# Optimization experiments

Measured on AMD Instinct MI355X. Metric: run time of the kernel, lower is better.

Reference implementation:

```python
import jax, jax.numpy as jnp
import numpy as np

B, S, D = 2, 2048, 4096
H, KVH, HD = 32, 8, 128
MULT = 0.08838834764831845  # 1/sqrt(head_dim)
MAXV = 30.0                 # tanh soft-cap
ROPE_BASE = 10000.0


def _rope_cos_sin(position_ids, hd=HD, base=ROPE_BASE):
    inv_freq = 1.0 / (base ** (jnp.arange(0, hd, 2, dtype=jnp.float32) / hd))
    freqs = position_ids.astype(jnp.float32)[..., None] * inv_freq  # [B,S,hd/2]
    emb = jnp.concatenate([freqs, freqs], axis=-1)                  # [B,S,hd]
    return jnp.cos(emb), jnp.sin(emb)


def _rotate_half(x):
    half = x.shape[-1] // 2
    return jnp.concatenate([-x[..., half:], x[..., :half]], axis=-1)


def setup_inputs() -> dict:
    key = jax.random.key(0)
    ks = jax.random.split(key, 5)
    hidden_states = jax.random.normal(ks[0], (B, S, D), dtype=jnp.float32)
    position_ids = jnp.broadcast_to(jnp.arange(S, dtype=jnp.int64), (B, S))
    # True = masked (causal upper triangle)
    causal = jnp.triu(jnp.ones((S, S), dtype=bool), k=1)
    attention_mask = jnp.broadcast_to(causal, (B, 1, S, S))
    sc = 0.02
    q_w = jax.random.normal(ks[1], (D, H * HD), dtype=jnp.float32) * sc
    k_w = jax.random.normal(ks[2], (D, KVH * HD), dtype=jnp.float32) * sc
    v_w = jax.random.normal(ks[3], (D, KVH * HD), dtype=jnp.float32) * sc
    o_w = jax.random.normal(ks[4], (H * HD, D), dtype=jnp.float32) * sc
    return {"hidden_states": hidden_states, "position_ids": position_ids,
            "attention_mask": attention_mask, "q_w": q_w, "k_w": k_w,
            "v_w": v_w, "o_w": o_w}


def reference(hidden_states, position_ids, attention_mask, q_w, k_w, v_w, o_w):
    bsz, q_len, _ = hidden_states.shape
    q = (hidden_states @ q_w).reshape(bsz, q_len, H, HD).transpose(0, 2, 1, 3)    # [B,H,S,HD]
    k = (hidden_states @ k_w).reshape(bsz, q_len, KVH, HD).transpose(0, 2, 1, 3)  # [B,KVH,S,HD]
    v = (hidden_states @ v_w).reshape(bsz, q_len, KVH, HD).transpose(0, 2, 1, 3)

    cos, sin = _rope_cos_sin(position_ids)   # [B,S,HD]
    cos = cos[:, None]                       # [B,1,S,HD]
    sin = sin[:, None]
    q = q * cos + _rotate_half(q) * sin
    k = k * cos + _rotate_half(k) * sin

    groups = H // KVH
    k = jnp.repeat(k, groups, axis=1)        # [B,H,S,HD]
    v = jnp.repeat(v, groups, axis=1)

    scores = jnp.einsum('bhqd,bhkd->bhqk', q, k).astype(jnp.float32) * MULT
    scores = MAXV * jnp.tanh(scores / MAXV)
    scores = jnp.where(attention_mask, jnp.float32(-10000.0), scores)
    attn = jax.nn.softmax(scores, axis=-1).astype(q.dtype)

    out = jnp.einsum('bhqk,bhkd->bhqd', attn, v)       # [B,H,S,HD]
    out = out.transpose(0, 2, 1, 3).reshape(bsz, q_len, H * HD)
    return out @ o_w
```

## Files before the change

kernel.cpp:

```cpp
#include <hip/hip_runtime.h>
#include <stdint.h>

#define B_ 2
#define S_ 2048
#define D_ 4096
#define H_ 32
#define KVH_ 8
#define HD_ 128
#define GRP_ (H_/KVH_)
#define NQKV 6144
#define MULT_ 0.08838834764831845f
#define MAXV_ 30.0f

typedef __attribute__((ext_vector_type(8))) short s16x8;
typedef __attribute__((ext_vector_type(4))) float fx4;

__device__ __forceinline__ unsigned short f2bf(float f) {
  unsigned int u = __float_as_uint(f);
  u += 0x7fffu + ((u >> 16) & 1u);
  return (unsigned short)(u >> 16);
}
__device__ __forceinline__ float bf2f(unsigned short h) {
  return __uint_as_float(((unsigned int)h) << 16);
}

__device__ __forceinline__ void gld_lds16(const void* g, void* l) {
  __builtin_amdgcn_global_load_lds(
      (const __attribute__((address_space(1))) unsigned int*)g,
      (__attribute__((address_space(3))) unsigned int*)l, 16, 0, 0);
}


__global__ void k_f2bf(const float* __restrict__ src, unsigned short* __restrict__ dst, int n4) {
  int i = blockIdx.x * blockDim.x + threadIdx.x;
  int stride = gridDim.x * blockDim.x;
  for (; i < n4; i += stride) {
    float4 v = ((const float4*)src)[i];
    ushort4 o;
    o.x = f2bf(v.x); o.y = f2bf(v.y); o.z = f2bf(v.z); o.w = f2bf(v.w);
    ((ushort4*)dst)[i] = o;
  }
}

__global__ void k_transpose_w(const float* __restrict__ src, int ncols,
                              unsigned short* __restrict__ dst) {
  __shared__ float tile[32][33];
  int k0 = blockIdx.x * 32;
  int n0 = blockIdx.y * 32;
  int tx = threadIdx.x, ty = threadIdx.y;
  for (int i = 0; i < 32; i += 8)
    tile[ty + i][tx] = src[(size_t)(k0 + ty + i) * ncols + n0 + tx];
  __syncthreads();
  for (int i = 0; i < 32; i += 8)
    dst[(size_t)(n0 + ty + i) * 4096 + k0 + tx] = f2bf(tile[tx][ty + i]);
}

__global__ void k_transpose_v(const unsigned short* __restrict__ qkv,
                              unsigned short* __restrict__ vt) {
  __shared__ unsigned short tile[32][33];
  int s0 = blockIdx.x * 32;
  int d0 = blockIdx.y * 32;
  int bk = blockIdx.z;
  int b = bk / KVH_, kvh = bk % KVH_;
  int tx = threadIdx.x, ty = threadIdx.y;
  for (int i = 0; i < 32; i += 8)
    tile[ty + i][tx] = qkv[(size_t)(b*S_ + s0 + ty + i)*NQKV + 5120 + kvh*HD_ + d0 + tx];
  __syncthreads();
  for (int i = 0; i < 32; i += 8)
    vt[((size_t)bk*HD_ + d0 + ty + i)*S_ + s0 + tx] = tile[tx][ty + i];
}

__global__ void k_rope(const unsigned short* __restrict__ qkv,
                       unsigned short* __restrict__ Q, unsigned short* __restrict__ K) {
  int bs = blockIdx.x;
  int b = bs >> 11;
  int s = bs & (S_ - 1);
  __shared__ float cs[64], sn[64];
  int t = threadIdx.x;
  if (t < 64) {
    float inv = __expf(-(float)t * 0.14391156831212787f);
    float fr = (float)s * inv;
    cs[t] = cosf(fr); sn[t] = sinf(fr);
  }
  __syncthreads();
  const unsigned short* row = qkv + (size_t)bs * NQKV;
  for (int i = t; i < H_*HD_; i += 256) {
    int h = i >> 7, d = i & 127;
    float x = bf2f(row[i]);
    float x2, c, si;
    if (d < 64) { x2 = -bf2f(row[h*128 + d + 64]); c = cs[d];    si = sn[d]; }
    else        { x2 =  bf2f(row[h*128 + d - 64]); c = cs[d-64]; si = sn[d-64]; }
    Q[((size_t)(b*H_ + h)*S_ + s)*HD_ + d] = f2bf(x*c + x2*si);
  }
  for (int i = t; i < KVH_*HD_; i += 256) {
    int h = i >> 7, d = i & 127;
    float x = bf2f(row[4096 + i]);
    float x2, c, si;
    if (d < 64) { x2 = -bf2f(row[4096 + h*128 + d + 64]); c = cs[d];    si = sn[d]; }
    else        { x2 =  bf2f(row[4096 + h*128 + d - 64]); c = cs[d-64]; si = sn[d-64]; }
    K[((size_t)(b*KVH_ + h)*S_ + s)*HD_ + d] = f2bf(x*c + x2*si);
  }
}

#define BAR() asm volatile("s_barrier" ::: "memory")
#define SB0() __builtin_amdgcn_sched_barrier(0)


#define STG4(buf, isB, h, kt) do {                                           \
  const unsigned short* _src = (isB) ? Bt : A;                               \
  size_t _rb = (size_t)(((isB) ? bn : bm)*((isB) ? 128 : 256)                \
                        + (h)*((isB) ? 64 : 128));                           \
  _Pragma("unroll") for (int _rr = 0; _rr < ((isB) ? 1 : 2); ++_rr) {        \
    int _s = _rr*8 + wv;                                                     \
    gld_lds16(_src + (_rb + (size_t)((_s>>1)*16))*Kd                         \
                   + (size_t)((kt)*64 + (_s&1)*32) + lane_off,               \
              ldsc + (buf)*49152 + (isB)*32768                               \
                   + (h)*((isB) ? 8192 : 16384) + _s*1024);                  \
  }                                                                          \
} while (0)

#define LDA4(buf, mh) do {                                                   \
  _Pragma("unroll") for (int _i = 0; _i < 4; ++_i)                           \
  _Pragma("unroll") for (int _kk = 0; _kk < 2; ++_kk)                        \
    Afr[_i*2+_kk] = *(const s16x8*)(ldsc + (buf)*49152 + wr*16384            \
                    + ((((mh)*4+_i)*2+_kk)*1024) + aswz);                    \
} while (0)

#define LDB4(buf) do {                                                       \
  _Pragma("unroll") for (int _nf = 0; _nf < 2; ++_nf)                        \
  _Pragma("unroll") for (int _kk = 0; _kk < 2; ++_kk) {                      \
    int _r0 = wc*32 + _nf*16;                                                \
    Bfr[_nf*2+_kk] = *(const s16x8*)(ldsc + (buf)*49152 + 32768              \
                    + (_r0>>6)*8192 + ((((_r0&63)>>4)*2+_kk)*1024) + aswz);  \
  }                                                                          \
} while (0)

#define MFMA16(MH) do {                                                      \
  __builtin_amdgcn_s_setprio(1);                                            \
  _Pragma("unroll") for (int _i = 0; _i < 4; ++_i)                           \
  _Pragma("unroll") for (int _nf = 0; _nf < 2; ++_nf)                        \
  _Pragma("unroll") for (int _kk = 0; _kk < 2; ++_kk)                        \
    acc[(MH)*4+_i][_nf] = __builtin_amdgcn_mfma_f32_16x16x32_bf16(           \
        Afr[_i*2+_kk], Bfr[_nf*2+_kk], acc[(MH)*4+_i][_nf], 0, 0, 0);        \
  __builtin_amdgcn_s_setprio(0);                                            \
} while (0)

#define VMC2() asm volatile("s_waitcnt vmcnt(2)" ::: "memory")

__global__ __launch_bounds__(512, 2)
void k_gemm4(const unsigned short* __restrict__ A, const unsigned short* __restrict__ Bt,
             unsigned short* __restrict__ C, int Kdim, int N, int MB) {
  __shared__ __align__(16) char ldsbuf[98304];
  char* ldsc = ldsbuf;
  const size_t Kd = (size_t)Kdim;
  const int NT = Kdim >> 6;

  int nwg = gridDim.x;
  int flat = blockIdx.x;
  int q = nwg >> 3, r8 = nwg & 7, xcd = flat & 7, off = flat >> 3;
  int wg = (xcd < r8 ? xcd*(q+1) : r8*(q+1) + (xcd-r8)*q) + off;
  int bm = wg % MB, bn = wg / MB;

  int tid = threadIdx.x;
  int lane = tid & 63, wv = tid >> 6;
  int wr = wv >> 2, wc = wv & 3;
  int l15 = lane & 15, l4 = lane >> 4;
  const int aswz = (l15 << 6) + ((l4 << 4) ^ ((l15 & 8) ? 32 : 0));
  const size_t lane_off = (size_t)(lane >> 2) * Kd
                        + (size_t)(((lane & 3) << 3) ^ ((lane & 32) >> 1));

  fx4 acc[8][2] = {};
  s16x8 Afr[8], Bfr[4];

  STG4(0, 0, 0, 0); STG4(0, 0, 1, 0);
  STG4(0, 1, 0, 0); STG4(0, 1, 1, 0);
  STG4(1, 1, 0, 1); STG4(1, 1, 1, 1);
  VMC2();
  BAR();

  for (int t2 = 0; t2 < NT; t2 += 2) {
    int tb1 = t2 + 1;
    int tn0 = t2 + 2; if (tn0 >= NT) tn0 -= NT;
    int tn1 = t2 + 3; if (tn1 >= NT) tn1 -= NT;
    LDA4(0, 0); LDB4(0);
    STG4(1, 0, 0, tb1); STG4(1, 0, 1, tb1);
    BAR();
    MFMA16(0);
    SB0(); BAR();
    LDA4(0, 1);
    STG4(0, 1, 0, tn0); STG4(0, 1, 1, tn0);
    BAR();
    MFMA16(1);
    SB0(); VMC2(); BAR();
    LDA4(1, 0); LDB4(1);
    STG4(0, 0, 0, tn0); STG4(0, 0, 1, tn0);
    BAR();
    MFMA16(0);
    SB0(); BAR();
    LDA4(1, 1);
    STG4(1, 1, 0, tn1); STG4(1, 1, 1, tn1);
    BAR();
    MFMA16(1);
    SB0(); VMC2(); BAR();
  }

  int m0 = bm*256 + wr*128 + l4*4;
#pragma unroll
  for (int af = 0; af < 8; ++af)
#pragma unroll
    for (int nf = 0; nf < 2; ++nf)
#pragma unroll
      for (int r = 0; r < 4; ++r) {
        int m = m0 + af*16 + r;
        int n = bn*128 + wc*32 + nf*16 + l15;
        C[(size_t)m*N + n] = f2bf(acc[af][nf][r]);
      }
}


#define STAGE(buf, isB, h, kt) do {                                          \
  const unsigned short* _src = (isB) ? Bt : A;                               \
  size_t _rb = (size_t)(((isB) ? bn : bm)*256 + (h)*128);                    \
  _Pragma("unroll") for (int _rr = 0; _rr < 2; ++_rr) {                      \
    int _s = _rr*8 + wv;                                                     \
    gld_lds16(_src + (_rb + (size_t)((_s>>1)*16))*Kd                         \
                   + (size_t)((kt)*64 + (_s&1)*32) + lane_off,               \
              ldsc + (buf)*65536 + (isB)*32768 + (h)*16384 + _s*1024);       \
  }                                                                          \
} while (0)

#define LDA(dst, buf, mh) do {                                               \
  _Pragma("unroll") for (int _i = 0; _i < 4; ++_i)                           \
  _Pragma("unroll") for (int _kk = 0; _kk < 2; ++_kk)                        \
    dst[_i*2+_kk] = *(const s16x8*)(ldsc + (buf)*65536 + wr*16384            \
                    + ((((mh)*4+_i)*2+_kk)*1024) + aswz);                    \
} while (0)

#define LDB(dst, buf, nh) do {                                               \
  _Pragma("unroll") for (int _j = 0; _j < 2; ++_j)                           \
  _Pragma("unroll") for (int _kk = 0; _kk < 2; ++_kk)                        \
    dst[_j*2+_kk] = *(const s16x8*)(ldsc + (buf)*65536 + 32768               \
                    + (wc>>1)*16384                                          \
                    + ((((wc&1)*4+(nh)*2+_j)*2+_kk)*1024) + aswz);           \
} while (0)

#define MFMA_Q(Aa, Bb, MH, NH) do {                                          \
  __builtin_amdgcn_s_setprio(1);                                            \
  _Pragma("unroll") for (int _i = 0; _i < 4; ++_i)                           \
  _Pragma("unroll") for (int _j = 0; _j < 2; ++_j)                           \
  _Pragma("unroll") for (int _kk = 0; _kk < 2; ++_kk)                        \
    acc[(MH)*4+_i][(NH)*2+_j] = __builtin_amdgcn_mfma_f32_16x16x32_bf16(     \
        Aa[_i*2+_kk], Bb[_j*2+_kk], acc[(MH)*4+_i][(NH)*2+_j], 0, 0, 0);     \
  __builtin_amdgcn_s_setprio(0);                                            \
} while (0)

#define VMC4() asm volatile("s_waitcnt vmcnt(4)" ::: "memory")

__global__ __launch_bounds__(512, 2)
void k_gemm8(const unsigned short* __restrict__ A, const unsigned short* __restrict__ Bt,
             float* __restrict__ C, int Kdim, int N, int MB) {
  __shared__ __align__(16) char ldsbuf[131072];
  char* ldsc = ldsbuf;
  const size_t Kd = (size_t)Kdim;
  const int NT = Kdim >> 6;

  int nwg = gridDim.x;
  int flat = blockIdx.x;
  int q = nwg >> 3, r8 = nwg & 7, xcd = flat & 7, off = flat >> 3;
  int wg = (xcd < r8 ? xcd*(q+1) : r8*(q+1) + (xcd-r8)*q) + off;
  int bm = wg % MB, bn = wg / MB;

  int tid = threadIdx.x;
  int lane = tid & 63, wv = tid >> 6;
  int wr = wv >> 2, wc = wv & 3;
  int l15 = lane & 15, l4 = lane >> 4;
  const int aswz = (l15 << 6) + ((l4 << 4) ^ ((l15 & 8) ? 32 : 0));
  const size_t lane_off = (size_t)(lane >> 2) * Kd
                        + (size_t)(((lane & 3) << 3) ^ ((lane & 32) >> 1));

  fx4 acc[8][4] = {};
  s16x8 Afr[8], B0fr[4], B1fr[4];

  STAGE(0, 0, 0, 0); STAGE(0, 0, 1, 0);
  STAGE(0, 1, 0, 0); STAGE(0, 1, 1, 0);
  STAGE(1, 1, 0, 1); STAGE(1, 1, 1, 1);
  VMC4();
  BAR();

  for (int t2 = 0; t2 < NT; t2 += 2) {
    int tb1 = t2 + 1;
    int tn0 = t2 + 2; if (tn0 >= NT) tn0 -= NT;
    int tn1 = t2 + 3; if (tn1 >= NT) tn1 -= NT;
    LDA(Afr, 0, 0); LDB(B0fr, 0, 0);
    STAGE(1, 0, 0, tb1);
    BAR();
    MFMA_Q(Afr, B0fr, 0, 0);
    SB0(); BAR();
    LDB(B1fr, 0, 1);
    STAGE(1, 0, 1, tb1);
    BAR();
    MFMA_Q(Afr, B1fr, 0, 1);
    SB0(); BAR();
    LDA(Afr, 0, 1);
    STAGE(0, 1, 0, tn0);
    BAR();
    MFMA_Q(Afr, B1fr, 1, 1);
    SB0(); BAR();
    STAGE(0, 1, 1, tn0);
    BAR();
    MFMA_Q(Afr, B0fr, 1, 0);
    SB0(); VMC4(); BAR();
    LDA(Afr, 1, 0); LDB(B0fr, 1, 0);
    STAGE(0, 0, 0, tn0);
    BAR();
    MFMA_Q(Afr, B0fr, 0, 0);
    SB0(); BAR();
    LDB(B1fr, 1, 1);
    STAGE(0, 0, 1, tn0);
    BAR();
    MFMA_Q(Afr, B1fr, 0, 1);
    SB0(); BAR();
    LDA(Afr, 1, 1);
    STAGE(1, 1, 0, tn1);
    BAR();
    MFMA_Q(Afr, B1fr, 1, 1);
    SB0(); BAR();
    STAGE(1, 1, 1, tn1);
    BAR();
    MFMA_Q(Afr, B0fr, 1, 0);
    SB0(); VMC4(); BAR();
  }

  int m0 = bm*256 + wr*128 + l4*4;
#pragma unroll
  for (int mf = 0; mf < 8; ++mf)
#pragma unroll
    for (int nf = 0; nf < 4; ++nf)
#pragma unroll
      for (int r = 0; r < 4; ++r) {
        int m = m0 + mf*16 + r;
        int n = bn*256 + (wc>>1)*128 + ((wc&1)*4 + nf)*16 + l15;
        C[(size_t)m*N + n] = acc[mf][nf][r];
      }
}


__global__ __launch_bounds__(256)
void k_attn8(const unsigned short* __restrict__ Q, const unsigned short* __restrict__ K,
             const unsigned short* __restrict__ Vt, unsigned short* __restrict__ Aout) {
  __shared__ unsigned short k_lds[2][32*128];
  __shared__ unsigned short v_lds[2][128*32];
  const float C1 = MULT_ * 2.0f * 1.4426950408889634f / MAXV_;
  const float C3 = 2.0f * MAXV_ * 1.4426950408889634f;
  int tpair = blockIdx.x;
  int bh = blockIdx.y;
  int b = bh >> 5, h = bh & 31;
  int kvh = h >> 2;
  int tid = threadIdx.x, lane = tid & 63, wv = tid >> 6;
  int l15 = lane & 15, l4 = lane >> 4;
  const unsigned short* Qb = Q + (size_t)bh * S_ * HD_;
  const unsigned short* Kb = K + (size_t)(b*KVH_ + kvh) * S_ * HD_;
  const unsigned short* Vb = Vt + (size_t)(b*KVH_ + kvh) * HD_ * S_;

  s16x8 ones;
#pragma unroll
  for (int i = 0; i < 8; ++i) ones[i] = (short)0x3F80;

#define STAGE_KV32(bufi, kb32) do {                                          \
  _Pragma("unroll") for (int _it = 0; _it < 2; ++_it) {                      \
    int _c = _it*256 + tid;                                                  \
    int _kr = _c >> 4;                                                       \
    int _kd = ((_c & 15) ^ (_kr & 7)) * 8;                                   \
    gld_lds16(&Kb[(size_t)((kb32) + _kr)*HD_ + _kd],                         \
              &k_lds[bufi][_it*2048 + wv*512]);                              \
    int _vd = _c >> 2;                                                       \
    int _vk = ((_c & 3) ^ (_vd & 3)) * 8;                                    \
    gld_lds16(&Vb[(size_t)_vd*S_ + (kb32) + _vk],                            \
              &v_lds[bufi][_it*2048 + wv*512]);                              \
  }                                                                          \
} while (0)

  for (int sp = 0; sp < 2; ++sp) {
    int strip = sp ? (31 - tpair) : tpair;
    int q0 = strip * 64;
    int qbase = q0 + wv * 16;
    int qr = qbase + l15;
    s16x8 bq[4];
#pragma unroll
    for (int kb = 0; kb < 4; ++kb)
      bq[kb] = *(const s16x8*)&Qb[(size_t)qr*HD_ + kb*32 + l4*8];
    fx4 oacc[8] = {};
    fx4 osum = {};
    int nt_full = qbase >> 5;
    int nt = (q0 >> 5) + 2;

    auto body = [&](int bufi, int kbase, bool domask) {
      fx4 sst[2] = {};
      __builtin_amdgcn_s_setprio(1);
#pragma unroll
      for (int nb = 0; nb < 2; ++nb)
#pragma unroll
        for (int kb = 0; kb < 4; ++kb) {
          s16x8 kf = *(const s16x8*)&k_lds[bufi][(nb*16 + l15)*128 + (((kb*4 + l4) ^ (l15 & 7)) * 8)];
          sst[nb] = __builtin_amdgcn_mfma_f32_16x16x32_bf16(kf, bq[kb], sst[nb], 0, 0, 0);
        }
      __builtin_amdgcn_s_setprio(0);
      uint32_t w[4];
#pragma unroll
      for (int nb = 0; nb < 2; ++nb) {
        float pv[4];
#pragma unroll
        for (int r = 0; r < 4; ++r) {
          float sraw = sst[nb][r];
          float e2p = __builtin_amdgcn_exp2f(sraw * C1);
          float p = __builtin_amdgcn_exp2f(-C3 * __builtin_amdgcn_rcpf(1.f + e2p));
          if (domask) {
            int kk = kbase + nb*16 + l4*4 + r;
            p = (kk <= qr) ? p : 0.f;
          }
          pv[r] = p;
        }
        w[nb*2]   = __builtin_amdgcn_perm(__float_as_uint(pv[1]), __float_as_uint(pv[0]), 0x07060302u);
        w[nb*2+1] = __builtin_amdgcn_perm(__float_as_uint(pv[3]), __float_as_uint(pv[2]), 0x07060302u);
      }
      uint32_t a0x = __shfl_xor((int)w[0], 16), a1x = __shfl_xor((int)w[1], 16);
      uint32_t b0x = __shfl_xor((int)w[2], 16), b1x = __shfl_xor((int)w[3], 16);
      bool up = (l4 & 1);
      uint32_t VA0 = up ? a0x : w[0], VA1 = up ? a1x : w[1];
      uint32_t VA2 = up ? w[0] : a0x, VA3 = up ? w[1] : a1x;
      uint32_t VB0 = up ? b0x : w[2], VB1 = up ? b1x : w[3];
      uint32_t VB2 = up ? w[2] : b0x, VB3 = up ? w[3] : b1x;
      bool lowh = (l4 < 2);
      uint32_t X0 = lowh ? VB0 : VA0, X1 = lowh ? VB1 : VA1;
      uint32_t X2 = lowh ? VB2 : VA2, X3 = lowh ? VB3 : VA3;
      uint32_t Y0 = __shfl_xor((int)X0, 32), Y1 = __shfl_xor((int)X1, 32);
      uint32_t Y2 = __shfl_xor((int)X2, 32), Y3 = __shfl_xor((int)X3, 32);
      union { uint32_t u[4]; s16x8 v; } tw;
      tw.u[0] = (l4 == 0) ? VA0 : (l4 == 3) ? VB0 : Y0;
      tw.u[1] = (l4 == 0) ? VA1 : (l4 == 3) ? VB1 : Y1;
      tw.u[2] = (l4 == 0) ? VA2 : (l4 == 3) ? VB2 : Y2;
      tw.u[3] = (l4 == 0) ? VA3 : (l4 == 3) ? VB3 : Y3;
      s16x8 pf = tw.v;
      __builtin_amdgcn_s_setprio(1);
      osum = __builtin_amdgcn_mfma_f32_16x16x32_bf16(ones, pf, osum, 0, 0, 0);
#pragma unroll
      for (int db = 0; db < 8; ++db) {
        int d = db*16 + l15;
        s16x8 vf = *(const s16x8*)&v_lds[bufi][d*32 + ((l4 ^ (d & 3)) * 8)];
        oacc[db] = __builtin_amdgcn_mfma_f32_16x16x32_bf16(vf, pf, oacc[db], 0, 0, 0);
      }
      __builtin_amdgcn_s_setprio(0);
    };

    STAGE_KV32(0, 0);
    __syncthreads();
    for (int t = 0; t < nt; ++t) {
      int bufi = t & 1;
      if (t + 1 < nt) STAGE_KV32(bufi^1, (t+1)*32);
      if (t < nt_full)       body(bufi, t*32, false);
      else if (t == nt_full) body(bufi, t*32, true);
      __syncthreads();
    }

    float rn = __builtin_amdgcn_rcpf(osum[0]);
#pragma unroll
    for (int db = 0; db < 8; ++db) {
      ushort4 o;
      o.x = f2bf(oacc[db][0] * rn);
      o.y = f2bf(oacc[db][1] * rn);
      o.z = f2bf(oacc[db][2] * rn);
      o.w = f2bf(oacc[db][3] * rn);
      *(ushort4*)&Aout[(size_t)(b*S_ + qr)*4096 + h*HD_ + db*16 + l4*4] = o;
    }
  }
#undef STAGE_KV32
}


extern "C" void kernel_launch(void* const* d_in, const int* in_sizes, int n_in,
                              void* d_out, int out_size, void* d_ws, size_t ws_size,
                              hipStream_t stream) {
  (void)in_sizes; (void)n_in; (void)out_size; (void)ws_size;
  const float* hidden = (const float*)d_in[0];
  const float* q_w = (const float*)d_in[3];
  const float* k_w = (const float*)d_in[4];
  const float* v_w = (const float*)d_in[5];
  const float* o_w = (const float*)d_in[6];
  char* ws = (char*)d_ws;
  unsigned short* hidden_bf = (unsigned short*)(ws + 0);
  unsigned short* qkv_wt    = (unsigned short*)(ws + 33554432);
  unsigned short* o_wt      = (unsigned short*)(ws + 83886080);
  unsigned short* qkv       = (unsigned short*)(ws + 117440512);
  unsigned short* Qb        = (unsigned short*)(ws + 167772160);
  unsigned short* Kb        = (unsigned short*)(ws + 201326592);
  unsigned short* Vt        = (unsigned short*)(ws + 209715200);
  unsigned short* attn_out  = (unsigned short*)(ws + 218103808);

  dim3 tb(32, 8);
  k_f2bf<<<2048, 256, 0, stream>>>(hidden, hidden_bf, (B_*S_*D_)/4);
  k_transpose_w<<<dim3(128, 128), tb, 0, stream>>>(q_w, 4096, qkv_wt);
  k_transpose_w<<<dim3(128, 32),  tb, 0, stream>>>(k_w, 1024, qkv_wt + (size_t)4096*4096);
  k_transpose_w<<<dim3(128, 32),  tb, 0, stream>>>(v_w, 1024, qkv_wt + (size_t)5120*4096);
  k_transpose_w<<<dim3(128, 128), tb, 0, stream>>>(o_w, 4096, o_wt);
  k_gemm4<<<dim3(16*48), 512, 0, stream>>>(hidden_bf, qkv_wt, qkv, D_, NQKV, 16);
  k_rope<<<B_*S_, 256, 0, stream>>>(qkv, Qb, Kb);
  k_transpose_v<<<dim3(S_/32, HD_/32, B_*KVH_), tb, 0, stream>>>(qkv, Vt);
  k_attn8<<<dim3(16, 64), 256, 0, stream>>>(Qb, Kb, Vt, attn_out);
  k_gemm8<<<dim3(16*16), 512, 0, stream>>>(attn_out, o_wt, (float*)d_out, D_, D_, 16);
}
```

Measured before the change: 582.4 us.

## Triple-buffer LDS staging in QKV projection GEMM with rotating buffers

Replaces the two-buffer, two-tiles-per-iteration pipeline of the QKV GEMM with a three-buffer LDS ring that prefetches two K-tiles ahead. Buffer indices rotate each iteration, and the wait changes to vmcnt(6), leaving one full tile of global loads in flight across the barrier. The goal is to hide more global-load latency behind the MFMA work. In exchange, LDS use grows to 144KB per block, which rules out any chance of two blocks per CU, and there is extra loop-control overhead per iteration.

```diff
diff --git a/kernel.cpp b/kernel.cpp
--- a/kernel.cpp
+++ b/kernel.cpp
@@ -104,6 +104,8 @@
 
 #define BAR() asm volatile("s_barrier" ::: "memory")
 #define SB0() __builtin_amdgcn_sched_barrier(0)
+#define VMC6() asm volatile("s_waitcnt vmcnt(6)" ::: "memory")
+#define VMC4() asm volatile("s_waitcnt vmcnt(4)" ::: "memory")
 
 
 #define STG4(buf, isB, h, kt) do {                                           \
@@ -145,12 +147,10 @@
   __builtin_amdgcn_s_setprio(0);                                            \
 } while (0)
 
-#define VMC2() asm volatile("s_waitcnt vmcnt(2)" ::: "memory")
-
 __global__ __launch_bounds__(512, 2)
-void k_gemm4(const unsigned short* __restrict__ A, const unsigned short* __restrict__ Bt,
-             unsigned short* __restrict__ C, int Kdim, int N, int MB) {
-  __shared__ __align__(16) char ldsbuf[98304];
+void k_gemm4t(const unsigned short* __restrict__ A, const unsigned short* __restrict__ Bt,
+              unsigned short* __restrict__ C, int Kdim, int N, int MB) {
+  __shared__ __align__(16) char ldsbuf[147456];
   char* ldsc = ldsbuf;
   const size_t Kd = (size_t)Kdim;
   const int NT = Kdim >> 6;
@@ -172,36 +172,25 @@
   fx4 acc[8][2] = {};
   s16x8 Afr[8], Bfr[4];
 
-  STG4(0, 0, 0, 0); STG4(0, 0, 1, 0);
-  STG4(0, 1, 0, 0); STG4(0, 1, 1, 0);
-  STG4(1, 1, 0, 1); STG4(1, 1, 1, 1);
-  VMC2();
+  STG4(0, 0, 0, 0); STG4(0, 0, 1, 0); STG4(0, 1, 0, 0); STG4(0, 1, 1, 0);
+  STG4(1, 0, 0, 1); STG4(1, 0, 1, 1); STG4(1, 1, 0, 1); STG4(1, 1, 1, 1);
+  VMC6();
   BAR();
 
-  for (int t2 = 0; t2 < NT; t2 += 2) {
-    int tb1 = t2 + 1;
-    int tn0 = t2 + 2; if (tn0 >= NT) tn0 -= NT;
-    int tn1 = t2 + 3; if (tn1 >= NT) tn1 -= NT;
-    LDA4(0, 0); LDB4(0);
-    STG4(1, 0, 0, tb1); STG4(1, 0, 1, tb1);
+  int r0 = 0, r1 = 1, r2 = 2;
+  for (int t = 0; t < NT; ++t) {
+    int tp2 = t + 2; if (tp2 >= NT) tp2 -= NT;
+    LDA4(r0, 0); LDB4(r0);
+    STG4(r2, 0, 0, tp2); STG4(r2, 0, 1, tp2);
     BAR();
     MFMA16(0);
     SB0(); BAR();
-    LDA4(0, 1);
-    STG4(0, 1, 0, tn0); STG4(0, 1, 1, tn0);
+    LDA4(r0, 1);
+    STG4(r2, 1, 0, tp2); STG4(r2, 1, 1, tp2);
     BAR();
     MFMA16(1);
-    SB0(); VMC2(); BAR();
-    LDA4(1, 0); LDB4(1);
-    STG4(0, 0, 0, tn0); STG4(0, 0, 1, tn0);
-    BAR();
-    MFMA16(0);
-    SB0(); BAR();
-    LDA4(1, 1);
-    STG4(1, 1, 0, tn1); STG4(1, 1, 1, tn1);
-    BAR();
-    MFMA16(1);
-    SB0(); VMC2(); BAR();
+    SB0(); VMC6(); BAR();
+    int tmp = r0; r0 = r1; r1 = r2; r2 = tmp;
   }
 
   int m0 = bm*256 + wr*128 + l4*4;
@@ -253,8 +242,6 @@
         Aa[_i*2+_kk], Bb[_j*2+_kk], acc[(MH)*4+_i][(NH)*2+_j], 0, 0, 0);     \
   __builtin_amdgcn_s_setprio(0);                                            \
 } while (0)
-
-#define VMC4() asm volatile("s_waitcnt vmcnt(4)" ::: "memory")
 
 __global__ __launch_bounds__(512, 2)
 void k_gemm8(const unsigned short* __restrict__ A, const unsigned short* __restrict__ Bt,
@@ -502,7 +489,7 @@
   k_transpose_w<<<dim3(128, 32),  tb, 0, stream>>>(k_w, 1024, qkv_wt + (size_t)4096*4096);
   k_transpose_w<<<dim3(128, 32),  tb, 0, stream>>>(v_w, 1024, qkv_wt + (size_t)5120*4096);
   k_transpose_w<<<dim3(128, 128), tb, 0, stream>>>(o_w, 4096, o_wt);
-  k_gemm4<<<dim3(16*48), 512, 0, stream>>>(hidden_bf, qkv_wt, qkv, D_, NQKV, 16);
+  k_gemm4t<<<dim3(16*48), 512, 0, stream>>>(hidden_bf, qkv_wt, qkv, D_, NQKV, 16);
   k_rope<<<B_*S_, 256, 0, stream>>>(qkv, Qb, Kb);
   k_transpose_v<<<dim3(S_/32, HD_/32, B_*KVH_), tb, 0, stream>>>(qkv, Vt);
   k_attn8<<<dim3(16, 64), 256, 0, stream>>>(Qb, Kb, Vt, attn_out);
```

New measurement: 589.2 us. No clear change (+1.2%).
